# Performance work log

Measured on AMD Instinct MI355X. Metric: run time of the kernel, lower is better.

Reference implementation:

```python
import jax, jax.numpy as jnp
import numpy as np
from jax import lax

NH = 8          # num_heads
DK = 256        # depth_k
DV = 256        # depth_v
DKH = DK // NH  # per-head key depth
DVH = DV // NH  # per-head value depth


def setup_inputs() -> dict:
    key = jax.random.key(0)
    k1, k2, k3 = jax.random.split(key, 3)
    B, C, H, W = 8, 256, 32, 32
    x = jax.random.normal(k1, (B, C, H, W), dtype=jnp.float32)
    # fan-in scaled init (glorot-like) to keep conv outputs / attention logits sane
    conv_w = jax.random.normal(k2, (3, 3, 256, 256), dtype=jnp.float32) / np.sqrt(3 * 3 * 256)
    conv_b = jnp.zeros((256,), dtype=jnp.float32)
    attn_w = jax.random.normal(k3, (1, 1, 256, 768), dtype=jnp.float32) / np.sqrt(256)
    attn_b = jnp.zeros((768,), dtype=jnp.float32)
    return {"x": x, "conv_w": conv_w, "conv_b": conv_b, "attn_w": attn_w, "attn_b": attn_b}


def _conv2d_same(x, w, b):
    # x: (B,C,H,W), w: (kh,kw,Cin,Cout) -> (B,Cout,H,W)
    y = lax.conv_general_dilated(x, w, window_strides=(1, 1), padding="SAME",
                                 dimension_numbers=("NCHW", "HWIO", "NCHW"))
    return y + b[None, :, None, None]


def reference(x, conv_w, conv_b, attn_w, attn_b):
    B, C, H, W = x.shape
    HW = H * W

    # parallel conv branch: channels_out - depth_v = 256 output channels
    conv_out = _conv2d_same(x, conv_w, conv_b)

    # 1x1 conv producing K, Q, V (split order matches tf.split([dk, dk, dv]))
    kqv = _conv2d_same(x, attn_w, attn_b)
    k = kqv[:, :DK]
    q = kqv[:, DK:2 * DK] * (DKH ** -0.5)
    v = kqv[:, 2 * DK:]

    # (B, Nh, d, HW) per-head flattening; token axis = HW
    def heads(t, d):
        return t.reshape(B, NH, d, HW)

    qh, kh, vh = heads(q, DKH), heads(k, DKH), heads(v, DVH)

    # logits: (B, Nh, HW, HW)
    logits = jnp.einsum("bhdn,bhdm->bhnm", qh, kh)
    weights = jax.nn.softmax(logits, axis=-1)
    # attn: (B, Nh, HW, dvh)
    attn = jnp.einsum("bhnm,bhdm->bhnd", weights, vh)

    # combine heads: (B,Nh,H,W,dvh) -> channel order (nh, dvh) -> (B, depth_v, H, W)
    attn_out = attn.reshape(B, NH, H, W, DVH).transpose(0, 1, 4, 2, 3).reshape(B, DV, H, W)

    return jnp.concatenate([conv_out, attn_out], axis=1)
```

## Files before the change

### kernel.cpp

```cpp
#include <hip/hip_runtime.h>


typedef __attribute__((ext_vector_type(8))) short short8;
typedef __attribute__((ext_vector_type(4))) float f32x4;
typedef __attribute__((ext_vector_type(16))) float f32x16;
typedef unsigned short u16;

#define QSCALE 0.25503487629898483f

__device__ inline u16 f2bf(float f) {
  unsigned u = __builtin_bit_cast(unsigned, f);
  return (u16)((u + 0x7FFFu + ((u >> 16) & 1u)) >> 16);
}
__device__ inline unsigned pack2bf(float a, float b) {
  return (unsigned)f2bf(a) | ((unsigned)f2bf(b) << 16);
}
__device__ inline unsigned packP(float a, float b) {
  unsigned au = __builtin_bit_cast(unsigned, a) + 0x8000u;
  unsigned bu = __builtin_bit_cast(unsigned, b) + 0x8000u;
  return __builtin_amdgcn_perm(bu, au, 0x07060302u);
}

__global__ __launch_bounds__(256) void prep_kernel(const float* __restrict__ x,
                                                   const float* __restrict__ cw,
                                                   const float* __restrict__ aw,
                                                   u16* __restrict__ xT,
                                                   u16* __restrict__ WcT,
                                                   u16* __restrict__ WaT) {
  __shared__ float T[64][65];
  int bid = blockIdx.x, tid = threadIdx.x;

  if (bid < 128) {
    int b = bid >> 4, n0 = (bid & 15) * 64;
#pragma unroll
    for (int rep = 0; rep < 2; ++rep) {
      int flat = rep * 256 + tid;
      int n = flat & 63, cg = flat >> 6;
      const float* xs = x + b * 256 * 1024 + n0 + n;
#pragma unroll
      for (int q = 0; q < 4; ++q) {
        uint4 pk;
#pragma unroll
        for (int jj = 0; jj < 4; ++jj) {
          float a = xs[(cg * 32 + q * 8 + 2 * jj) * 1024];
          float c = xs[(cg * 32 + q * 8 + 2 * jj + 1) * 1024];
          ((unsigned*)&pk)[jj] = packP(a, c);
        }
        *(uint4*)&xT[(b * 1024 + n0 + n) * 256 + cg * 32 + q * 8] = pk;
      }
    }
    return;
  }

  int tt = bid - 128;
  int chunk = tt >> 4, t = tt & 15;
  int ci0 = (t & 3) * 64, r0 = (t >> 2) * 64;
  bool isconv = chunk < 9;
  float scale = (chunk == 10) ? QSCALE : 1.0f;

#pragma unroll
  for (int rep = 0; rep < 16; ++rep) {
    int flat = rep * 256 + tid;
    int i = flat >> 6, j = flat & 63;
    T[i][j] = isconv ? cw[(chunk * 256 + ci0 + i) * 256 + r0 + j]
                     : aw[(ci0 + i) * 768 + (chunk - 9) * 256 + r0 + j];
  }
  __syncthreads();
#pragma unroll
  for (int rep = 0; rep < 4; ++rep) {
    int flat = rep * 256 + tid;
    int jj = flat >> 4, qq = flat & 15;
    float v0 = T[qq * 4 + 0][jj] * scale;
    float v1 = T[qq * 4 + 1][jj] * scale;
    float v2 = T[qq * 4 + 2][jj] * scale;
    float v3 = T[qq * 4 + 3][jj] * scale;
    uint2 pk = {pack2bf(v0, v1), pack2bf(v2, v3)};
    if (isconv)
      *(uint2*)&WcT[(chunk * 256 + r0 + jj) * 256 + ci0 + qq * 4] = pk;
    else
      *(uint2*)&WaT[((chunk - 9) * 256 + r0 + jj) * 256 + ci0 + qq * 4] = pk;
  }
}

__global__ __launch_bounds__(256) void kqv_kernel(const u16* __restrict__ xT,
                                                  const u16* __restrict__ WaT,
                                                  const float* __restrict__ ab,
                                                  u16* __restrict__ kT,
                                                  u16* __restrict__ qT,
                                                  u16* __restrict__ vB) {
  __shared__ __align__(16) u16 S[15360];
  int bid = blockIdx.x;
  int b = bid & 7, idx = bid >> 3;
  int ot = idx >> 4, nt = idx & 15;
  int tid = threadIdx.x, wave = tid >> 6, lane = tid & 63;
  int ln = lane & 15, g = lane >> 4;
  int o0 = ot * 128 + (wave & 1) * 64;
  int n0 = nt * 64 + (wave >> 1) * 32;
  const u16* xb = xT + b * 1024 * 256;

  int rA = tid >> 2, slA = tid & 3;
  const u16* aS0 = WaT + (ot * 128 + rA) * 256 + slA * 8;
  const u16* aS1 = aS0 + 64 * 256;
  const u16* bS = xb + (nt * 64 + rA) * 256 + slA * 8;
  int aD0 = rA * 40 + slA * 8;
  int aD1 = aD0 + 64 * 40;
  int bD = 5120 + rA * 40 + slA * 8;

  int aF = ((wave & 1) * 64 + ln) * 40 + g * 8;
  int bF = 5120 + ((wave >> 1) * 32 + ln) * 40 + g * 8;

  f32x4 acc[4][2];
#pragma unroll
  for (int i = 0; i < 4; ++i)
#pragma unroll
    for (int j = 0; j < 2; ++j) acc[i][j] = (f32x4){0.f, 0.f, 0.f, 0.f};

  *(short8*)&S[aD0] = *(const short8*)aS0;
  *(short8*)&S[aD1] = *(const short8*)aS1;
  *(short8*)&S[bD] = *(const short8*)bS;
  __syncthreads();
  short8 pa0 = *(const short8*)(aS0 + 32);
  short8 pa1 = *(const short8*)(aS1 + 32);
  short8 pb = *(const short8*)(bS + 32);

#pragma unroll
  for (int s = 0; s < 8; ++s) {
    const u16* buf = S + (s & 1) * 7680;
    short8 a0 = *(const short8*)&buf[aF];
    short8 a1 = *(const short8*)&buf[aF + 16 * 40];
    short8 a2 = *(const short8*)&buf[aF + 32 * 40];
    short8 a3 = *(const short8*)&buf[aF + 48 * 40];
    short8 b0 = *(const short8*)&buf[bF];
    short8 b1 = *(const short8*)&buf[bF + 16 * 40];
    acc[0][0] = __builtin_amdgcn_mfma_f32_16x16x32_bf16(a0, b0, acc[0][0], 0, 0, 0);
    acc[0][1] = __builtin_amdgcn_mfma_f32_16x16x32_bf16(a0, b1, acc[0][1], 0, 0, 0);
    acc[1][0] = __builtin_amdgcn_mfma_f32_16x16x32_bf16(a1, b0, acc[1][0], 0, 0, 0);
    acc[1][1] = __builtin_amdgcn_mfma_f32_16x16x32_bf16(a1, b1, acc[1][1], 0, 0, 0);
    acc[2][0] = __builtin_amdgcn_mfma_f32_16x16x32_bf16(a2, b0, acc[2][0], 0, 0, 0);
    acc[2][1] = __builtin_amdgcn_mfma_f32_16x16x32_bf16(a2, b1, acc[2][1], 0, 0, 0);
    acc[3][0] = __builtin_amdgcn_mfma_f32_16x16x32_bf16(a3, b0, acc[3][0], 0, 0, 0);
    acc[3][1] = __builtin_amdgcn_mfma_f32_16x16x32_bf16(a3, b1, acc[3][1], 0, 0, 0);
    if (s < 7) {
      u16* nb = S + ((s + 1) & 1) * 7680;
      *(short8*)&nb[aD0] = pa0;
      *(short8*)&nb[aD1] = pa1;
      *(short8*)&nb[bD] = pb;
      if (s < 6) {
        pa0 = *(const short8*)(aS0 + (s + 2) * 32);
        pa1 = *(const short8*)(aS1 + (s + 2) * 32);
        pb = *(const short8*)(bS + (s + 2) * 32);
      }
    }
    __syncthreads();
  }

  if (ot >= 4) {
#pragma unroll
    for (int it = 0; it < 4; ++it)
#pragma unroll
      for (int r = 0; r < 4; ++r) {
        int o = o0 + it * 16 + g * 4 + r;
        float bias = ab[o];
#pragma unroll
        for (int jt = 0; jt < 2; ++jt) {
          int n = n0 + jt * 16 + ln;
          vB[(b * 256 + (o - 512)) * 1024 + n] = f2bf(acc[it][jt][r] + bias);
        }
      }
    return;
  }

  u16* Tt = S;
  bool isQ = (ot >= 2);
  float bs = isQ ? QSCALE : 1.0f;
  int olb = (wave & 1) * 64;
  int nlb = (wave >> 1) * 32;
#pragma unroll
  for (int it = 0; it < 4; ++it)
#pragma unroll
    for (int jt = 0; jt < 2; ++jt) {
      int ol = olb + it * 16 + g * 4;
      int nl = nlb + jt * 16 + ln;
      int og = ot * 128 + ol;
      float v0 = acc[it][jt][0] + ab[og + 0] * bs;
      float v1 = acc[it][jt][1] + ab[og + 1] * bs;
      float v2 = acc[it][jt][2] + ab[og + 2] * bs;
      float v3 = acc[it][jt][3] + ab[og + 3] * bs;
      uint2 pk = {pack2bf(v0, v1), pack2bf(v2, v3)};
      *(uint2*)&Tt[nl * 136 + ol] = pk;
    }
  __syncthreads();
  u16* dst = isQ ? qT : kT;
#pragma unroll
  for (int rep = 0; rep < 4; ++rep) {
    int flat = rep * 256 + tid;
    int o8 = flat & 15, nl = flat >> 4;
    short8 v = *(const short8*)&Tt[nl * 136 + o8 * 8];
    int og256 = (ot & 1) * 128 + o8 * 8;
    int hh = og256 >> 5, d0 = og256 & 31;
    int ng = nt * 64 + nl;
    *(short8*)&dst[((b * 8 + hh) * 1024 + ng) * 32 + d0] = v;
  }
}

__global__ __launch_bounds__(256, 3) void conv_attn_kernel(
    const u16* __restrict__ xT, const u16* __restrict__ WcT,
    const float* __restrict__ cb, const u16* __restrict__ kT,
    const u16* __restrict__ qT, const u16* __restrict__ vB,
    float* __restrict__ out) {
  __shared__ __align__(16) unsigned char smem[19584];

  int bid = blockIdx.x;
  int b = bid & 7;
  int sub = bid >> 3;
  int trip = sub / 3;
  int rem = sub - trip * 3;
  int tid = threadIdx.x;
  int wave = tid >> 6, lane = tid & 63;

  if (rem == 2) {
    int ln = lane & 15, g = lane >> 4;
    u16* Xc = (u16*)smem;
    int hp = trip >> 1, coh = trip & 1;
    int h0 = hp * 2;
    int co0 = coh * 128 + wave * 32;

    f32x4 acc[2][4];
#pragma unroll
    for (int i = 0; i < 2; ++i)
#pragma unroll
      for (int j = 0; j < 4; ++j) acc[i][j] = (f32x4){0.f, 0.f, 0.f, 0.f};

    {
      int rp = tid >> 6, rest = tid & 63;
      int which = rest >> 5, cp = rest & 31;
      *(unsigned*)&Xc[(rp * 34 + which * 33) * 72 + cp * 2] = 0u;
    }

    for (int c0 = 0; c0 < 256; c0 += 64) {
      __syncthreads();
#pragma unroll
      for (int rep = 0; rep < 4; ++rep) {
        int flat = rep * 256 + tid;
        int cg = flat & 7, w = (flat >> 3) & 31, rp = flat >> 8;
        int row = h0 - 1 + rp;
        short8 v = {0, 0, 0, 0, 0, 0, 0, 0};
        if ((unsigned)row < 32u)
          v = *(const short8*)&xT[(b * 1024 + row * 32 + w) * 256 + c0 + cg * 8];
        int rowS = rp * 34 + w + 1;
        *(short8*)&Xc[rowS * 72 + ((cg ^ (rowS & 7)) * 8)] = v;
      }
      __syncthreads();
#pragma unroll
      for (int ks = 0; ks < 2; ++ks) {
        int ko = c0 + ks * 32 + g * 8;
        int slot = ks * 4 + g;
#pragma unroll
        for (int r = 0; r < 3; ++r)
#pragma unroll
          for (int s = 0; s < 3; ++s) {
            int tap = r * 3 + s;
            short8 a0 = *(const short8*)&WcT[(tap * 256 + co0 + ln) * 256 + ko];
            short8 a1 =
                *(const short8*)&WcT[(tap * 256 + co0 + 16 + ln) * 256 + ko];
#pragma unroll
            for (int jt = 0; jt < 4; ++jt) {
              int rowp = ((jt >> 1) + r) * 34 + (jt & 1) * 16 + ln + s;
              short8 bf =
                  *(const short8*)&Xc[rowp * 72 + ((slot ^ (rowp & 7)) * 8)];
              acc[0][jt] = __builtin_amdgcn_mfma_f32_16x16x32_bf16(
                  a0, bf, acc[0][jt], 0, 0, 0);
              acc[1][jt] = __builtin_amdgcn_mfma_f32_16x16x32_bf16(
                  a1, bf, acc[1][jt], 0, 0, 0);
            }
          }
      }
    }

#pragma unroll
    for (int it = 0; it < 2; ++it)
#pragma unroll
      for (int r4 = 0; r4 < 4; ++r4) {
        int co = co0 + it * 16 + g * 4 + r4;
        float bias = cb[co];
#pragma unroll
        for (int jt = 0; jt < 4; ++jt) {
          int h = h0 + (jt >> 1), w = (jt & 1) * 16 + ln;
          out[((b * 512 + co) * 32 + h) * 32 + w] = acc[it][jt][r4] + bias;
        }
      }
    return;
  }

  u16* kvb = (u16*)smem;
  int idx = trip * 2 + rem;
  int h = idx >> 3, qt = idx & 7;
  int nw = qt * 128 + wave * 32;
  int lq = lane & 31, hi = lane >> 5;

  const u16* kb = kT + (b * 8 + h) * (1024 * 32);
  const u16* qb = qT + (b * 8 + h) * (1024 * 32);
  const u16* vb = vB + (b * 256 + h * 32) * 1024;

  short8 qf0 = *(const short8*)&qb[(nw + lq) * 32 + hi * 8];
  short8 qf1 = *(const short8*)&qb[(nw + lq) * 32 + 16 + hi * 8];

  int sr = tid >> 2, ss = tid & 3;
  int dvr = tid >> 3, vs = tid & 7;
  const u16* ksrc = kb + sr * 32 + ss * 8;
  const u16* vsrc = vb + dvr * 1024 + vs * 8;
  int kdst = sr * 40 + ss * 8;
  int vdst = 2560 + dvr * 72 + vs * 8;

  int kr0 = lq * 40;
  int kr1 = (32 + lq) * 40;
  int vr = 2560 + lq * 72;

  f32x16 o0a = {}, o0b = {};
  float mx = -1e30f, l = 0.f;

  short8 kp = *(const short8*)ksrc;
  short8 vp = *(const short8*)vsrc;
  *(short8*)&kvb[kdst] = kp;
  *(short8*)&kvb[vdst] = vp;
  __syncthreads();
  kp = *(const short8*)(ksrc + 2048);
  vp = *(const short8*)(vsrc + 64);

  for (int mt = 0; mt < 16; ++mt) {
    u16* bc = kvb + (mt & 1) * 4864;
    if (mt < 15) {
      u16* bn = kvb + ((mt + 1) & 1) * 4864;
      *(short8*)&bn[kdst] = kp;
      *(short8*)&bn[vdst] = vp;
    }
    if (mt < 14) {
      kp = *(const short8*)(ksrc + (mt + 2) * 2048);
      vp = *(const short8*)(vsrc + (mt + 2) * 64);
    }

    short8 ka00 = *(const short8*)&bc[kr0 + hi * 8];
    short8 ka01 = *(const short8*)&bc[kr0 + 16 + hi * 8];
    short8 ka10 = *(const short8*)&bc[kr1 + hi * 8];
    short8 ka11 = *(const short8*)&bc[kr1 + 16 + hi * 8];
    f32x16 s0t = {}, s1t = {};
    __builtin_amdgcn_s_setprio(1);
    s0t = __builtin_amdgcn_mfma_f32_32x32x16_bf16(ka00, qf0, s0t, 0, 0, 0);
    s1t = __builtin_amdgcn_mfma_f32_32x32x16_bf16(ka10, qf0, s1t, 0, 0, 0);
    s0t = __builtin_amdgcn_mfma_f32_32x32x16_bf16(ka01, qf1, s0t, 0, 0, 0);
    s1t = __builtin_amdgcn_mfma_f32_32x32x16_bf16(ka11, qf1, s1t, 0, 0, 0);
    __builtin_amdgcn_s_setprio(0);

    short8 vf0 = *(const short8*)&bc[vr + hi * 8];
    short8 vf1 = *(const short8*)&bc[vr + 16 + hi * 8];
    short8 vf2 = *(const short8*)&bc[vr + 32 + hi * 8];
    short8 vf3 = *(const short8*)&bc[vr + 48 + hi * 8];

    float tmax = s0t[0];
#pragma unroll
    for (int r = 1; r < 16; ++r) tmax = fmaxf(tmax, s0t[r]);
#pragma unroll
    for (int r = 0; r < 16; ++r) tmax = fmaxf(tmax, s1t[r]);
    tmax = fmaxf(tmax, __shfl_xor(tmax, 32));

    if (!__all(tmax - mx <= 8.0f)) {
      float nm = fmaxf(mx, tmax);
      float sc = __builtin_amdgcn_exp2f(mx - nm);
#pragma unroll
      for (int r = 0; r < 16; ++r) {
        o0a[r] *= sc;
        o0b[r] *= sc;
      }
      l *= sc;
      mx = nm;
    }

#pragma unroll
    for (int r = 0; r < 16; ++r) {
      s0t[r] = __builtin_amdgcn_exp2f(s0t[r] - mx);
      s1t[r] = __builtin_amdgcn_exp2f(s1t[r] - mx);
    }
    float ts = 0.f;
#pragma unroll
    for (int r = 0; r < 16; ++r) ts += s0t[r] + s1t[r];
    ts += __shfl_xor(ts, 32);
    l += ts;

    __builtin_amdgcn_s_setprio(1);
#define PV_CHUNK(SV, CB, VF, ACC)                                             \
  {                                                                           \
    unsigned A0 = packP(SV[(CB) + 0], SV[(CB) + 1]);                          \
    unsigned A1 = packP(SV[(CB) + 2], SV[(CB) + 3]);                          \
    unsigned B0 = packP(SV[(CB) + 4], SV[(CB) + 5]);                          \
    unsigned B1 = packP(SV[(CB) + 6], SV[(CB) + 7]);                          \
    unsigned sm0 = hi ? A0 : B0, sm1 = hi ? A1 : B1;                          \
    unsigned r0_ = (unsigned)__shfl_xor((int)sm0, 32);                        \
    unsigned r1_ = (unsigned)__shfl_xor((int)sm1, 32);                        \
    uint4 fw;                                                                 \
    fw.x = hi ? r0_ : A0;                                                     \
    fw.y = hi ? r1_ : A1;                                                     \
    fw.z = hi ? B0 : r0_;                                                     \
    fw.w = hi ? B1 : r1_;                                                     \
    short8 pf = __builtin_bit_cast(short8, fw);                               \
    ACC = __builtin_amdgcn_mfma_f32_32x32x16_bf16(VF, pf, ACC, 0, 0, 0);      \
  }
    PV_CHUNK(s0t, 0, vf0, o0a)
    PV_CHUNK(s0t, 8, vf1, o0b)
    PV_CHUNK(s1t, 0, vf2, o0a)
    PV_CHUNK(s1t, 8, vf3, o0b)
#undef PV_CHUNK
    __builtin_amdgcn_s_setprio(0);

    __syncthreads();
  }

  float rl = 1.f / l;
  float* ob = out + (b * 512 + 256 + h * 32) * 1024 + nw + lq;
#pragma unroll
  for (int r = 0; r < 16; ++r) {
    int dv = (r & 3) + 8 * (r >> 2) + 4 * hi;
    ob[dv * 1024] = (o0a[r] + o0b[r]) * rl;
  }
}

extern "C" void kernel_launch(void* const* d_in, const int* in_sizes, int n_in,
                              void* d_out, int out_size, void* d_ws,
                              size_t ws_size, hipStream_t stream) {
  const float* x  = (const float*)d_in[0];
  const float* cw = (const float*)d_in[1];
  const float* cb = (const float*)d_in[2];
  const float* aw = (const float*)d_in[3];
  const float* ab = (const float*)d_in[4];
  float* out = (float*)d_out;

  char* ws = (char*)d_ws;
  u16* vB  = (u16*)ws;
  u16* kT  = (u16*)(ws + 4194304);
  u16* qT  = (u16*)(ws + 8388608);
  u16* xT  = (u16*)(ws + 12582912);
  u16* WcT = (u16*)(ws + 16777216);
  u16* WaT = (u16*)(ws + 17956864);

  prep_kernel<<<320, 256, 0, stream>>>(x, cw, aw, xT, WcT, WaT);
  kqv_kernel<<<768, 256, 0, stream>>>(xT, WaT, ab, kT, qT, vB);
  conv_attn_kernel<<<768, 256, 0, stream>>>(xT, WcT, cb, kT, qT, vB, out);
}
```

Before: 54.58 us.

## Software-pipeline QK MFMA one tile ahead with 4-stage LDS ring

The attention loop now computes the QK scores for the next K/V tile before doing the softmax and PV work for the current tile, so matrix-core work overlaps the exp and reduction stages. The LDS K/V buffer grows from double to a four-slot ring, which allows one barrier per iteration placed after the stores instead of at the loop end. This raises shared memory per block to about 38 KB, which may lower occupancy for the three-blocks-per-CU launch bound, and adds register pressure from holding two sets of score accumulators.

```diff
diff --git a/kernel.cpp b/kernel.cpp
--- a/kernel.cpp
+++ b/kernel.cpp
@@ -208,7 +208,7 @@
     const float* __restrict__ cb, const u16* __restrict__ kT,
     const u16* __restrict__ qT, const u16* __restrict__ vB,
     float* __restrict__ out) {
-  __shared__ __align__(16) unsigned char smem[19584];
+  __shared__ __align__(16) unsigned char smem[38912];
 
   int bid = blockIdx.x;
   int b = bid & 7;
@@ -323,44 +323,60 @@
   short8 vp = *(const short8*)vsrc;
   *(short8*)&kvb[kdst] = kp;
   *(short8*)&kvb[vdst] = vp;
-  __syncthreads();
   kp = *(const short8*)(ksrc + 2048);
   vp = *(const short8*)(vsrc + 64);
-
-  for (int mt = 0; mt < 16; ++mt) {
-    u16* bc = kvb + (mt & 1) * 4864;
-    if (mt < 15) {
-      u16* bn = kvb + ((mt + 1) & 1) * 4864;
+  __syncthreads();
+
+  f32x16 sc0 = {}, sc1 = {};
+  {
+    short8 ka00 = *(const short8*)&kvb[kr0 + hi * 8];
+    short8 ka01 = *(const short8*)&kvb[kr0 + 16 + hi * 8];
+    short8 ka10 = *(const short8*)&kvb[kr1 + hi * 8];
+    short8 ka11 = *(const short8*)&kvb[kr1 + 16 + hi * 8];
+    sc0 = __builtin_amdgcn_mfma_f32_32x32x16_bf16(ka00, qf0, sc0, 0, 0, 0);
+    sc1 = __builtin_amdgcn_mfma_f32_32x32x16_bf16(ka10, qf0, sc1, 0, 0, 0);
+    sc0 = __builtin_amdgcn_mfma_f32_32x32x16_bf16(ka01, qf1, sc0, 0, 0, 0);
+    sc1 = __builtin_amdgcn_mfma_f32_32x32x16_bf16(ka11, qf1, sc1, 0, 0, 0);
+  }
+
+#pragma unroll 4
+  for (int t = 0; t < 16; ++t) {
+    u16* bn = kvb + ((t + 1) & 3) * 4864;
+    const u16* bcur = kvb + (t & 3) * 4864;
+    if (t < 15) {
       *(short8*)&bn[kdst] = kp;
       *(short8*)&bn[vdst] = vp;
     }
-    if (mt < 14) {
-      kp = *(const short8*)(ksrc + (mt + 2) * 2048);
-      vp = *(const short8*)(vsrc + (mt + 2) * 64);
-    }
-
-    short8 ka00 = *(const short8*)&bc[kr0 + hi * 8];
-    short8 ka01 = *(const short8*)&bc[kr0 + 16 + hi * 8];
-    short8 ka10 = *(const short8*)&bc[kr1 + hi * 8];
-    short8 ka11 = *(const short8*)&bc[kr1 + 16 + hi * 8];
-    f32x16 s0t = {}, s1t = {};
-    __builtin_amdgcn_s_setprio(1);
-    s0t = __builtin_amdgcn_mfma_f32_32x32x16_bf16(ka00, qf0, s0t, 0, 0, 0);
-    s1t = __builtin_amdgcn_mfma_f32_32x32x16_bf16(ka10, qf0, s1t, 0, 0, 0);
-    s0t = __builtin_amdgcn_mfma_f32_32x32x16_bf16(ka01, qf1, s0t, 0, 0, 0);
-    s1t = __builtin_amdgcn_mfma_f32_32x32x16_bf16(ka11, qf1, s1t, 0, 0, 0);
-    __builtin_amdgcn_s_setprio(0);
-
-    short8 vf0 = *(const short8*)&bc[vr + hi * 8];
-    short8 vf1 = *(const short8*)&bc[vr + 16 + hi * 8];
-    short8 vf2 = *(const short8*)&bc[vr + 32 + hi * 8];
-    short8 vf3 = *(const short8*)&bc[vr + 48 + hi * 8];
-
-    float tmax = s0t[0];
-#pragma unroll
-    for (int r = 1; r < 16; ++r) tmax = fmaxf(tmax, s0t[r]);
-#pragma unroll
-    for (int r = 0; r < 16; ++r) tmax = fmaxf(tmax, s1t[r]);
+    if (t < 14) {
+      kp = *(const short8*)(ksrc + (t + 2) * 2048);
+      vp = *(const short8*)(vsrc + (t + 2) * 64);
+    }
+    __syncthreads();
+
+    f32x16 sn0 = {}, sn1 = {};
+    if (t < 15) {
+      __builtin_amdgcn_s_setprio(1);
+      short8 ka00 = *(const short8*)&bn[kr0 + hi * 8];
+      short8 ka01 = *(const short8*)&bn[kr0 + 16 + hi * 8];
+      short8 ka10 = *(const short8*)&bn[kr1 + hi * 8];
+      short8 ka11 = *(const short8*)&bn[kr1 + 16 + hi * 8];
+      sn0 = __builtin_amdgcn_mfma_f32_32x32x16_bf16(ka00, qf0, sn0, 0, 0, 0);
+      sn1 = __builtin_amdgcn_mfma_f32_32x32x16_bf16(ka10, qf0, sn1, 0, 0, 0);
+      sn0 = __builtin_amdgcn_mfma_f32_32x32x16_bf16(ka01, qf1, sn0, 0, 0, 0);
+      sn1 = __builtin_amdgcn_mfma_f32_32x32x16_bf16(ka11, qf1, sn1, 0, 0, 0);
+      __builtin_amdgcn_s_setprio(0);
+    }
+
+    short8 vf0 = *(const short8*)&bcur[vr + hi * 8];
+    short8 vf1 = *(const short8*)&bcur[vr + 16 + hi * 8];
+    short8 vf2 = *(const short8*)&bcur[vr + 32 + hi * 8];
+    short8 vf3 = *(const short8*)&bcur[vr + 48 + hi * 8];
+
+    float tmax = sc0[0];
+#pragma unroll
+    for (int r = 1; r < 16; ++r) tmax = fmaxf(tmax, sc0[r]);
+#pragma unroll
+    for (int r = 0; r < 16; ++r) tmax = fmaxf(tmax, sc1[r]);
     tmax = fmaxf(tmax, __shfl_xor(tmax, 32));
 
     if (!__all(tmax - mx <= 8.0f)) {
@@ -377,12 +393,12 @@
 
 #pragma unroll
     for (int r = 0; r < 16; ++r) {
-      s0t[r] = __builtin_amdgcn_exp2f(s0t[r] - mx);
-      s1t[r] = __builtin_amdgcn_exp2f(s1t[r] - mx);
+      sc0[r] = __builtin_amdgcn_exp2f(sc0[r] - mx);
+      sc1[r] = __builtin_amdgcn_exp2f(sc1[r] - mx);
     }
     float ts = 0.f;
 #pragma unroll
-    for (int r = 0; r < 16; ++r) ts += s0t[r] + s1t[r];
+    for (int r = 0; r < 16; ++r) ts += sc0[r] + sc1[r];
     ts += __shfl_xor(ts, 32);
     l += ts;
 
@@ -404,14 +420,15 @@
     short8 pf = __builtin_bit_cast(short8, fw);                               \
     ACC = __builtin_amdgcn_mfma_f32_32x32x16_bf16(VF, pf, ACC, 0, 0, 0);      \
   }
-    PV_CHUNK(s0t, 0, vf0, o0a)
-    PV_CHUNK(s0t, 8, vf1, o0b)
-    PV_CHUNK(s1t, 0, vf2, o0a)
-    PV_CHUNK(s1t, 8, vf3, o0b)
+    PV_CHUNK(sc0, 0, vf0, o0a)
+    PV_CHUNK(sc0, 8, vf1, o0b)
+    PV_CHUNK(sc1, 0, vf2, o0a)
+    PV_CHUNK(sc1, 8, vf3, o0b)
 #undef PV_CHUNK
     __builtin_amdgcn_s_setprio(0);
 
-    __syncthreads();
+    sc0 = sn0;
+    sc1 = sn1;
   }
 
   float rl = 1.f / l;
```

New measurement: 54.61 us (median of 2 runs). Within noise of the previous version (+0.1%).
